# Kernel optimization log

Measured on AMD Instinct MI355X. Metric: run time of the kernel, lower is better.

The kernel has to match this reference:

```python
import jax, jax.numpy as jnp
import numpy as np

B, S, D, H = 1, 4096, 768, 12
Dh = D // H  # 64


def setup_inputs() -> dict:
    key = jax.random.key(0)
    ks = jax.random.split(key, 11)
    w = lambda k, sh: jax.random.normal(k, sh, jnp.float32) * 0.02
    return {
        "query": jax.random.normal(ks[0], (B, S, D), jnp.float32),
        "key": jax.random.normal(ks[1], (B, S, D), jnp.float32),
        "value": jax.random.normal(ks[2], (B, S, D), jnp.float32),
        "mask": jnp.ones((B, S), jnp.int32),  # nonzero = attend; mask==0 positions are filled with -inf
        "Wq": w(ks[3], (D, D)), "bq": w(ks[4], (D,)),
        "Wk": w(ks[5], (D, D)), "bk": w(ks[6], (D,)),
        "Wv": w(ks[7], (D, D)), "bv": w(ks[8], (D,)),
        "Wo": w(ks[9], (D, D)), "bo": w(ks[10], (D,)),
    }


def reference(query, key, value, mask, Wq, bq, Wk, bk, Wv, bv, Wo, bo):
    # shape(): (B, S, D) -> (B, H, S, Dh)
    def split_heads(x):
        return x.reshape(B, S, H, Dh).transpose(0, 2, 1, 3)

    q = split_heads(query @ Wq.T + bq) / np.sqrt(Dh).astype(np.float32)
    k = split_heads(key @ Wk.T + bk)
    # multi_rand_attn_cuda is an unbiased randomized estimator of
    # weights @ v_lin(value); the exact-math baseline applies v_lin then
    # contracts with the attention weights per head.
    v = split_heads(value @ Wv.T + bv)

    scores = jnp.einsum('bhqd,bhkd->bhqk', q, k)  # (B,H,S,S)
    scores = jnp.where((mask == 0)[:, None, None, :], -jnp.inf, scores)
    weights = jax.nn.softmax(scores, axis=-1)  # dropout is identity at eval

    ctx = jnp.einsum('bhqk,bhkd->bhqd', weights, v)
    ctx = ctx.transpose(0, 2, 1, 3).reshape(B, S, D)  # unshape
    return ctx @ Wo.T + bo
```

## Files before the change

### kernel.cpp

```cpp
#include <hip/hip_runtime.h>

#define S_LEN 4096
#define D_MODEL 768
#define N_HEADS 12
#define D_HEAD 64

typedef short bf16x8 __attribute__((ext_vector_type(8)));
typedef float f32x4 __attribute__((ext_vector_type(4)));
typedef float f32x16 __attribute__((ext_vector_type(16)));
typedef float f32x4v __attribute__((ext_vector_type(4)));
typedef unsigned short u16;
typedef unsigned short u16x8 __attribute__((ext_vector_type(8)));
typedef unsigned int u32;

__device__ __forceinline__ u16 f2bf(float f) {
  unsigned u = __float_as_uint(f);
  u += 0x7FFFu + ((u >> 16) & 1u);
  return (u16)(u >> 16);
}

__device__ __forceinline__ u32 pk2bf(float lo, float hi) {
  u32 a = __float_as_uint(hi) + 0x8000u;
  u32 b = __float_as_uint(lo) + 0x8000u;
  return __builtin_amdgcn_perm(a, b, 0x07060302u);
}

__device__ __forceinline__ void gl_lds16(const void* g, void* l) {
  __builtin_amdgcn_global_load_lds(
      (const __attribute__((address_space(1))) void*)g,
      (__attribute__((address_space(3))) void*)l, 16, 0, 0);
}

struct CvtArgs7 {
  const float* s[7];
  u16* d[7];
  long n[7];
};

__global__ __launch_bounds__(256) void cvt8_kernel(CvtArgs7 a) {
  const int z = blockIdx.z;
  const float* s = a.s[z];
  u16* d = a.d[z];
  long i = ((long)blockIdx.x * 256 + threadIdx.x) * 8;
  if (i >= a.n[z]) return;
  f32x4v v0 = *(const f32x4v*)(s + i);
  f32x4v v1 = *(const f32x4v*)(s + i + 4);
  u16x8 o;
#pragma unroll
  for (int j = 0; j < 4; ++j) { o[j] = f2bf(v0[j]); o[j + 4] = f2bf(v1[j]); }
  *(u16x8*)(d + i) = o;
}

struct ProjArgs {
  const u16* A[3];
  const u16* W[3];
  const float* bias[3];
  void* out[3];
  float scale[3];
  int mode[3];
};

template <int TM>
__global__ __launch_bounds__(256, 2) void proj_kernel(ProjArgs args) {
  constexpr int MF = TM / 32;
  constexpr int CA = TM / 16;
  const int z = blockIdx.z;
  const u16* __restrict__ A = args.A[z];
  const u16* __restrict__ W = args.W[z];
  const float* __restrict__ bias = args.bias[z];
  const float scale = args.scale[z];
  const int mode = args.mode[z];

  __shared__ u16 Al[TM * 32];
  __shared__ u16 Bl[128 * 32];
  __shared__ u16 Ep[TM == 128 ? 16384 : 1];

  const int tid = threadIdx.x;
  const int w = tid >> 6, l = tid & 63;
  const int l15 = l & 15, quad = l >> 4;
  const int m0 = blockIdx.x * TM;
  const int n0 = blockIdx.y * 128;
  const int wm = (w & 1) * (TM / 2), wn = (w >> 1) * 64;
  const int crow = l >> 2, ccol = (l & 3) * 8;

  f32x4 acc[MF][4] = {};

  for (int kt = 0; kt < 24; ++kt) {
    const int k0 = kt * 32;
#pragma unroll
    for (int i = 0; i < CA / 4; ++i) {
      const int sub = w * (CA / 4) + i;
      const int row = sub * 16 + crow;
      gl_lds16(&A[(size_t)(m0 + row) * D_MODEL + k0 + ccol], &Al[sub * 512 + l * 8]);
    }
#pragma unroll
    for (int i = 0; i < 2; ++i) {
      const int sub = w * 2 + i;
      const int row = sub * 16 + crow;
      gl_lds16(&W[(size_t)(n0 + row) * D_MODEL + k0 + ccol], &Bl[sub * 512 + l * 8]);
    }
    __syncthreads();
    bf16x8 af[MF], bfr[4];
#pragma unroll
    for (int mf = 0; mf < MF; ++mf)
      af[mf] = *(const bf16x8*)&Al[(wm + mf * 16 + l15) * 32 + quad * 8];
#pragma unroll
    for (int nf = 0; nf < 4; ++nf)
      bfr[nf] = *(const bf16x8*)&Bl[(wn + nf * 16 + l15) * 32 + quad * 8];
#pragma unroll
    for (int mf = 0; mf < MF; ++mf)
#pragma unroll
      for (int nf = 0; nf < 4; ++nf)
        acc[mf][nf] = __builtin_amdgcn_mfma_f32_16x16x32_bf16(af[mf], bfr[nf], acc[mf][nf], 0, 0, 0);
    __syncthreads();
  }

  if (mode == 3 || mode == 4) {
#pragma unroll
    for (int nf = 0; nf < 4; ++nf) {
      const float bv = bias[n0 + wn + nf * 16 + l15];
#pragma unroll
      for (int mf = 0; mf < MF; ++mf) {
#pragma unroll
        for (int r = 0; r < 4; ++r) {
          const float v = acc[mf][nf][r] + bv;
          int off;
          if (mode == 3) {
            off = (((w >> 1) * 16 + ((w & 1) * 2 + (mf >> 1)) * 4 + nf) << 9) +
                  (((l15 >> 3) * 32 + (mf & 1) * 16 + quad * 4 + r) << 3) + (l15 & 7);
          } else {
            off = (((w >> 1) * 16 + ((w & 1) * 2 + (mf >> 1)) * 4 + (nf >> 1) * 2 + (mf & 1)) << 9) +
                  (((quad & 1) * 32 + (nf & 1) * 16 + l15) << 3) + r + 4 * (quad >> 1);
          }
          Ep[off] = f2bf(v);
        }
      }
    }
    __syncthreads();
    const int hh0 = n0 >> 6, st0 = m0 >> 5;
    u16* outp = (u16*)args.out[z];
#pragma unroll
    for (int hloc = 0; hloc < 2; ++hloc) {
      u16* dst = outp + ((size_t)((hh0 + hloc) * 128 + st0) * 4) * 512;
#pragma unroll
      for (int c = 0; c < 4; ++c) {
        u16x8 v = *(u16x8*)&Ep[hloc * 8192 + w * 2048 + c * 512 + l * 8];
        *(u16x8*)(dst + w * 2048 + c * 512 + l * 8) = v;
      }
    }
  } else {
#pragma unroll
    for (int nf = 0; nf < 4; ++nf) {
      const int col = n0 + wn + nf * 16 + l15;
      const float bv = bias[col];
#pragma unroll
      for (int mf = 0; mf < MF; ++mf) {
#pragma unroll
        for (int r = 0; r < 4; ++r) {
          const int row = m0 + wm + mf * 16 + quad * 4 + r;
          const float v = (acc[mf][nf][r] + bv) * scale;
          if (mode == 0) ((u16*)args.out[z])[(size_t)row * D_MODEL + col] = f2bf(v);
          else           ((float*)args.out[z])[(size_t)row * D_MODEL + col] = v;
        }
      }
    }
  }
}

__global__ __launch_bounds__(256, 2) void flash_kernel(
    const u16* __restrict__ Qb, const u16* __restrict__ Kpk,
    const u16* __restrict__ Vpk, const int* __restrict__ mask,
    u16* __restrict__ Ctx) {
  __shared__ char smem[34816];

  const int tid = threadIdx.x;
  const int w = tid >> 6, l = tid & 63;
  const int l31 = l & 31, g = l >> 5;
  const int h = blockIdx.y;
  const int q0 = blockIdx.x * 64;

  bf16x8 qf[2][4];
#pragma unroll
  for (int qs = 0; qs < 2; ++qs) {
    const u16* qrow = Qb + (size_t)(q0 + qs * 32 + l31) * D_MODEL + h * D_HEAD + g * 8;
#pragma unroll
    for (int s = 0; s < 4; ++s) qf[qs][s] = *(const bf16x8*)(qrow + s * 16);
  }

  const u16* kb = Kpk + ((size_t)h * 128 + w * 32) * 2048 + l * 8;
  const u16* vb = Vpk + ((size_t)h * 128 + w * 32) * 2048 + l * 8;
  const int* mk = mask + w * 1024 + l31;

  f32x16 oacc[2][2] = {};
  float lsum[2] = {0.f, 0.f};

  bf16x8 kfA[4], vfA[4], kfB[4], vfB[4];
  int mvA, mvB;

  mvA = mk[0];
#pragma unroll
  for (int c = 0; c < 4; ++c) kfA[c] = *(const bf16x8*)(kb + c * 512);
#pragma unroll
  for (int c = 0; c < 4; ++c) vfA[c] = *(const bf16x8*)(vb + c * 512);

#define FLASH_COMPUTE(KF, VF, MV)                                              \
  {                                                                            \
    const unsigned long long mb = __ballot((MV) != 0);                         \
    _Pragma("unroll") for (int qs = 0; qs < 2; ++qs) {                         \
      f32x16 sacc = {};                                                        \
      _Pragma("unroll") for (int s = 0; s < 4; ++s)                            \
          sacc = __builtin_amdgcn_mfma_f32_32x32x16_bf16(KF[s], qf[qs][s],     \
                                                         sacc, 0, 0, 0);       \
      _Pragma("unroll") for (int r = 0; r < 16; ++r)                           \
          sacc[r] = __builtin_amdgcn_exp2f(sacc[r]);                           \
      if (mb + 1ull != 0ull) {                                                 \
        const unsigned mh = (unsigned)(mb >> (4 * g));                         \
        _Pragma("unroll") for (int r = 0; r < 16; ++r)                         \
            if (!((mh >> ((r & 3) + 8 * (r >> 2))) & 1u)) sacc[r] = 0.f;       \
      }                                                                        \
      float ts = 0.f;                                                          \
      _Pragma("unroll") for (int r = 0; r < 16; ++r) ts += sacc[r];            \
      lsum[qs] += ts;                                                          \
      u32 pk[8];                                                               \
      _Pragma("unroll") for (int i = 0; i < 8; ++i)                            \
          pk[i] = pk2bf(sacc[2 * i], sacc[2 * i + 1]);                         \
      _Pragma("unroll") for (int u = 0; u < 2; ++u) {                          \
        union { u32 u4[4]; bf16x8 s; } bp;                                     \
        _Pragma("unroll") for (int i = 0; i < 4; ++i) bp.u4[i] = pk[4 * u + i];\
        oacc[qs][0] = __builtin_amdgcn_mfma_f32_32x32x16_bf16(VF[u], bp.s,     \
                                                              oacc[qs][0], 0, 0, 0); \
        oacc[qs][1] = __builtin_amdgcn_mfma_f32_32x32x16_bf16(VF[2 + u], bp.s, \
                                                              oacc[qs][1], 0, 0, 0); \
      }                                                                        \
    }                                                                          \
  }

  for (int p = 0; p < 16; ++p) {
    {
      const int nt = 2 * p + 1;
      mvB = mk[nt * 32];
      const u16* kn = kb + (size_t)nt * 2048;
      const u16* vn = vb + (size_t)nt * 2048;
#pragma unroll
      for (int c = 0; c < 4; ++c) kfB[c] = *(const bf16x8*)(kn + c * 512);
#pragma unroll
      for (int c = 0; c < 4; ++c) vfB[c] = *(const bf16x8*)(vn + c * 512);
      FLASH_COMPUTE(kfA, vfA, mvA)
    }
    {
      const int nt = (2 * p + 2 < 32) ? 2 * p + 2 : 31;
      mvA = mk[nt * 32];
      const u16* kn = kb + (size_t)nt * 2048;
      const u16* vn = vb + (size_t)nt * 2048;
#pragma unroll
      for (int c = 0; c < 4; ++c) kfA[c] = *(const bf16x8*)(kn + c * 512);
#pragma unroll
      for (int c = 0; c < 4; ++c) vfA[c] = *(const bf16x8*)(vn + c * 512);
      FLASH_COMPUTE(kfB, vfB, mvB)
    }
  }
#undef FLASH_COMPUTE

  float* Ol = (float*)smem;
  float* Ll = (float*)(smem + 32768);
  Ll[w * 128 + l] = lsum[0];
  Ll[w * 128 + 64 + l] = lsum[1];
#pragma unroll
  for (int ph = 0; ph < 2; ++ph) {
    __syncthreads();
#pragma unroll
    for (int db = 0; db < 2; ++db)
#pragma unroll
      for (int r = 0; r < 16; ++r)
        Ol[((w * 2 + db) * 16 + r) * 64 + l] = oacc[ph][db][r];
    __syncthreads();

    float Lt = 0.f;
#pragma unroll
    for (int kq = 0; kq < 4; ++kq)
      Lt += Ll[kq * 128 + ph * 64 + l] + Ll[kq * 128 + ph * 64 + (l ^ 32)];
    const float linv = 1.0f / Lt;

    const int db = w & 1;
#pragma unroll
    for (int t = 0; t < 2; ++t) {
      const int rr = (w >> 1) * 2 + t;
      float v[4];
#pragma unroll
      for (int i = 0; i < 4; ++i) {
        const int r = rr * 4 + i;
        float acc = 0.f;
#pragma unroll
        for (int kq = 0; kq < 4; ++kq)
          acc += Ol[((kq * 2 + db) * 16 + r) * 64 + l];
        v[i] = acc * linv;
      }
      u16* cp = Ctx + (size_t)(q0 + ph * 32 + l31) * D_MODEL + h * D_HEAD + db * 32 + rr * 8 + 4 * g;
      *(u32*)(cp) = pk2bf(v[0], v[1]);
      *(u32*)(cp + 2) = pk2bf(v[2], v[3]);
    }
  }
}

extern "C" void kernel_launch(void* const* d_in, const int* in_sizes, int n_in,
                              void* d_out, int out_size, void* d_ws, size_t ws_size,
                              hipStream_t stream) {
  const float* query = (const float*)d_in[0];
  const float* key   = (const float*)d_in[1];
  const float* value = (const float*)d_in[2];
  const int*   maskp = (const int*)d_in[3];
  const float* Wq = (const float*)d_in[4];
  const float* bq = (const float*)d_in[5];
  const float* Wk = (const float*)d_in[6];
  const float* bk = (const float*)d_in[7];
  const float* Wv = (const float*)d_in[8];
  const float* bv = (const float*)d_in[9];
  const float* Wo = (const float*)d_in[10];
  const float* bo = (const float*)d_in[11];

  char* ws = (char*)d_ws;
  const size_t SZX = (size_t)S_LEN * D_MODEL * 2;
  const size_t SZW = (size_t)D_MODEL * D_MODEL * 2;
  u16* Xq  = (u16*)(ws);
  u16* Xk  = (u16*)(ws + SZX);
  u16* Xv  = (u16*)(ws + 2 * SZX);
  u16* Qb  = (u16*)(ws + 3 * SZX);
  u16* Kpk = (u16*)(ws + 4 * SZX);
  u16* Vpk = (u16*)(ws + 5 * SZX);
  u16* Wqb = (u16*)(ws + 6 * SZX);
  u16* Wkb = (u16*)(ws + 6 * SZX + SZW);
  u16* Wvb = (u16*)(ws + 6 * SZX + 2 * SZW);
  u16* Wob = (u16*)(ws + 6 * SZX + 3 * SZW);
  u16* Ctx = Xq;

  CvtArgs7 cc;
  cc.s[0] = query; cc.s[1] = key; cc.s[2] = value;
  cc.s[3] = Wq; cc.s[4] = Wk; cc.s[5] = Wv; cc.s[6] = Wo;
  cc.d[0] = Xq; cc.d[1] = Xk; cc.d[2] = Xv;
  cc.d[3] = Wqb; cc.d[4] = Wkb; cc.d[5] = Wvb; cc.d[6] = Wob;
  const long nact = (long)S_LEN * D_MODEL, nw = (long)D_MODEL * D_MODEL;
  cc.n[0] = cc.n[1] = cc.n[2] = nact;
  cc.n[3] = cc.n[4] = cc.n[5] = cc.n[6] = nw;
  cvt8_kernel<<<dim3(1536, 1, 7), 256, 0, stream>>>(cc);

  ProjArgs pa;
  pa.A[0] = Xq;  pa.A[1] = Xk;  pa.A[2] = Xv;
  pa.W[0] = Wqb; pa.W[1] = Wkb; pa.W[2] = Wvb;
  pa.bias[0] = bq; pa.bias[1] = bk; pa.bias[2] = bv;
  pa.out[0] = Qb; pa.out[1] = Kpk; pa.out[2] = Vpk;
  pa.scale[0] = 0.125f * 1.4426950408889634f; pa.scale[1] = 1.f; pa.scale[2] = 1.f;
  pa.mode[0] = 0; pa.mode[1] = 3; pa.mode[2] = 4;
  proj_kernel<128><<<dim3(32, 6, 3), 256, 0, stream>>>(pa);

  flash_kernel<<<dim3(64, N_HEADS, 1), 256, 0, stream>>>(Qb, Kpk, Vpk, maskp, Ctx);

  ProjArgs po;
  po.A[0] = Ctx; po.A[1] = Ctx; po.A[2] = Ctx;
  po.W[0] = Wob; po.W[1] = Wob; po.W[2] = Wob;
  po.bias[0] = bo; po.bias[1] = bo; po.bias[2] = bo;
  po.out[0] = d_out; po.out[1] = d_out; po.out[2] = d_out;
  po.scale[0] = 1.f; po.scale[1] = 1.f; po.scale[2] = 1.f;
  po.mode[0] = 2; po.mode[1] = 2; po.mode[2] = 2;
  proj_kernel<64><<<dim3(64, 6, 1), 256, 0, stream>>>(po);
}
```

Measured before the change: 210.4 us.

## Pre-pack weights into MFMA fragment layout and double-buffer A tiles in projection GEMM

The weight conversion kernel now writes bf16 weights in a tile-packed layout that matches the MFMA B-fragment order. The projection kernel can then load weight fragments straight from global memory into registers instead of staging them through LDS. The A tile is double-buffered in LDS, and the next weight fragments are prefetched into registers, which removes one barrier per k-step and overlaps loads with MFMA work. The cost is higher register pressure and weight reads that go to global/L2 without sharing across waves.

```diff
diff --git a/kernel.cpp b/kernel.cpp
--- a/kernel.cpp
+++ b/kernel.cpp
@@ -35,20 +35,35 @@
   const float* s[7];
   u16* d[7];
   long n[7];
+  int packw[7];
 };
 
 __global__ __launch_bounds__(256) void cvt8_kernel(CvtArgs7 a) {
   const int z = blockIdx.z;
   const float* s = a.s[z];
   u16* d = a.d[z];
-  long i = ((long)blockIdx.x * 256 + threadIdx.x) * 8;
-  if (i >= a.n[z]) return;
-  f32x4v v0 = *(const f32x4v*)(s + i);
-  f32x4v v1 = *(const f32x4v*)(s + i + 4);
-  u16x8 o;
-#pragma unroll
-  for (int j = 0; j < 4; ++j) { o[j] = f2bf(v0[j]); o[j + 4] = f2bf(v1[j]); }
-  *(u16x8*)(d + i) = o;
+  if (a.packw[z]) {
+    const int t = blockIdx.x * 256 + threadIdx.x;
+    if (t >= (int)a.n[z]) return;
+    const int nr = t / 96, o = t - nr * 96;
+    const float* src = s + (size_t)nr * D_MODEL + o * 8;
+    f32x4v v0 = *(const f32x4v*)(src);
+    f32x4v v1 = *(const f32x4v*)(src + 4);
+    u16x8 ov;
+#pragma unroll
+    for (int j = 0; j < 4; ++j) { ov[j] = f2bf(v0[j]); ov[j + 4] = f2bf(v1[j]); }
+    const int off = ((nr >> 4) * 24 + (o >> 2)) * 512 + ((o & 3) * 16 + (nr & 15)) * 8;
+    *(u16x8*)(d + off) = ov;
+  } else {
+    long i = ((long)blockIdx.x * 256 + threadIdx.x) * 8;
+    if (i >= a.n[z]) return;
+    f32x4v v0 = *(const f32x4v*)(s + i);
+    f32x4v v1 = *(const f32x4v*)(s + i + 4);
+    u16x8 ov;
+#pragma unroll
+    for (int j = 0; j < 4; ++j) { ov[j] = f2bf(v0[j]); ov[j + 4] = f2bf(v1[j]); }
+    *(u16x8*)(d + i) = ov;
+  }
 }
 
 struct ProjArgs {
@@ -63,16 +78,15 @@
 template <int TM>
 __global__ __launch_bounds__(256, 2) void proj_kernel(ProjArgs args) {
   constexpr int MF = TM / 32;
-  constexpr int CA = TM / 16;
+  constexpr int ISS = TM / 64;
   const int z = blockIdx.z;
   const u16* __restrict__ A = args.A[z];
-  const u16* __restrict__ W = args.W[z];
+  const u16* __restrict__ Wp = args.W[z];
   const float* __restrict__ bias = args.bias[z];
   const float scale = args.scale[z];
   const int mode = args.mode[z];
 
-  __shared__ u16 Al[TM * 32];
-  __shared__ u16 Bl[128 * 32];
+  __shared__ u16 Al[2][TM * 32];
   __shared__ u16 Ep[TM == 128 ? 16384 : 1];
 
   const int tid = threadIdx.x;
@@ -82,37 +96,48 @@
   const int n0 = blockIdx.y * 128;
   const int wm = (w & 1) * (TM / 2), wn = (w >> 1) * 64;
   const int crow = l >> 2, ccol = (l & 3) * 8;
+  const int ntb = (n0 >> 4) + (w >> 1) * 4;
 
   f32x4 acc[MF][4] = {};
-
+  bf16x8 wf[4], wfn[4];
+
+#pragma unroll
+  for (int nf = 0; nf < 4; ++nf)
+    wf[nf] = *(const bf16x8*)(Wp + (size_t)((ntb + nf) * 24 + 0) * 512 + l * 8);
+#pragma unroll
+  for (int i = 0; i < ISS; ++i) {
+    const int sub = w * ISS + i;
+    gl_lds16(&A[(size_t)(m0 + sub * 16 + crow) * D_MODEL + ccol], &Al[0][sub * 512 + l * 8]);
+  }
+
+  int buf = 0;
   for (int kt = 0; kt < 24; ++kt) {
-    const int k0 = kt * 32;
-#pragma unroll
-    for (int i = 0; i < CA / 4; ++i) {
-      const int sub = w * (CA / 4) + i;
-      const int row = sub * 16 + crow;
-      gl_lds16(&A[(size_t)(m0 + row) * D_MODEL + k0 + ccol], &Al[sub * 512 + l * 8]);
-    }
-#pragma unroll
-    for (int i = 0; i < 2; ++i) {
-      const int sub = w * 2 + i;
-      const int row = sub * 16 + crow;
-      gl_lds16(&W[(size_t)(n0 + row) * D_MODEL + k0 + ccol], &Bl[sub * 512 + l * 8]);
-    }
     __syncthreads();
-    bf16x8 af[MF], bfr[4];
+    if (kt < 23) {
+#pragma unroll
+      for (int i = 0; i < ISS; ++i) {
+        const int sub = w * ISS + i;
+        gl_lds16(&A[(size_t)(m0 + sub * 16 + crow) * D_MODEL + (kt + 1) * 32 + ccol],
+                 &Al[buf ^ 1][sub * 512 + l * 8]);
+      }
+#pragma unroll
+      for (int nf = 0; nf < 4; ++nf)
+        wfn[nf] = *(const bf16x8*)(Wp + (size_t)((ntb + nf) * 24 + kt + 1) * 512 + l * 8);
+    }
+    bf16x8 af[MF];
 #pragma unroll
     for (int mf = 0; mf < MF; ++mf)
-      af[mf] = *(const bf16x8*)&Al[(wm + mf * 16 + l15) * 32 + quad * 8];
-#pragma unroll
-    for (int nf = 0; nf < 4; ++nf)
-      bfr[nf] = *(const bf16x8*)&Bl[(wn + nf * 16 + l15) * 32 + quad * 8];
+      af[mf] = *(const bf16x8*)&Al[buf][(wm + mf * 16 + l15) * 32 + quad * 8];
 #pragma unroll
     for (int mf = 0; mf < MF; ++mf)
 #pragma unroll
       for (int nf = 0; nf < 4; ++nf)
-        acc[mf][nf] = __builtin_amdgcn_mfma_f32_16x16x32_bf16(af[mf], bfr[nf], acc[mf][nf], 0, 0, 0);
-    __syncthreads();
+        acc[mf][nf] = __builtin_amdgcn_mfma_f32_16x16x32_bf16(af[mf], wf[nf], acc[mf][nf], 0, 0, 0);
+    if (kt < 23) {
+#pragma unroll
+      for (int nf = 0; nf < 4; ++nf) wf[nf] = wfn[nf];
+    }
+    buf ^= 1;
   }
 
   if (mode == 3 || mode == 4) {
@@ -338,9 +363,11 @@
   cc.s[3] = Wq; cc.s[4] = Wk; cc.s[5] = Wv; cc.s[6] = Wo;
   cc.d[0] = Xq; cc.d[1] = Xk; cc.d[2] = Xv;
   cc.d[3] = Wqb; cc.d[4] = Wkb; cc.d[5] = Wvb; cc.d[6] = Wob;
-  const long nact = (long)S_LEN * D_MODEL, nw = (long)D_MODEL * D_MODEL;
+  const long nact = (long)S_LEN * D_MODEL;
   cc.n[0] = cc.n[1] = cc.n[2] = nact;
-  cc.n[3] = cc.n[4] = cc.n[5] = cc.n[6] = nw;
+  cc.n[3] = cc.n[4] = cc.n[5] = cc.n[6] = (long)D_MODEL * 96;
+  cc.packw[0] = cc.packw[1] = cc.packw[2] = 0;
+  cc.packw[3] = cc.packw[4] = cc.packw[5] = cc.packw[6] = 1;
   cvt8_kernel<<<dim3(1536, 1, 7), 256, 0, stream>>>(cc);
 
   ProjArgs pa;
```

After: 213.5 us. About the same (+1.5%).
